# Performance work log

Hardware: AMD Instinct MI355X
Metric: run time of the kernel (lower is better)

Reference implementation:

```python
import jax, jax.numpy as jnp
import numpy as np


def _lstm_cell(x, h, c, w_ih, w_hh, b_ih, b_hh):
    gates = x @ w_ih.T + b_ih + h @ w_hh.T + b_hh  # [B, 4H]
    i, f, g, o = jnp.split(gates, 4, axis=1)
    i = jax.nn.sigmoid(i)
    f = jax.nn.sigmoid(f)
    g = jnp.tanh(g)
    o = jax.nn.sigmoid(o)
    c_next = f * c + i * g
    h_next = o * jnp.tanh(c_next)
    return h_next, c_next


def setup_inputs() -> dict:
    key = jax.random.key(0)
    B, T, D_ENC, H, E, J, V = 32, 512, 512, 640, 640, 640, 4096
    ks = jax.random.split(key, 20)
    s = 0.05
    return {
        "encoder_outputs": jax.random.normal(ks[0], (B, D_ENC, T), jnp.float32),
        "targets": jax.random.randint(ks[1], (B, 1), 0, V, jnp.int64),
        "target_length": jnp.ones((B,), jnp.int32),
        "input_states_1": jax.random.normal(ks[2], (2, B, H), jnp.float32),
        "input_states_2": jax.random.normal(ks[3], (2, B, H), jnp.float32),
        "lstm_w_ih_l0": jax.random.normal(ks[4], (4 * H, E), jnp.float32) * s,
        "lstm_w_hh_l0": jax.random.normal(ks[5], (4 * H, H), jnp.float32) * s,
        "lstm_b_ih_l0": jax.random.normal(ks[6], (4 * H,), jnp.float32) * s,
        "lstm_b_hh_l0": jax.random.normal(ks[7], (4 * H,), jnp.float32) * s,
        "lstm_w_ih_l1": jax.random.normal(ks[8], (4 * H, H), jnp.float32) * s,
        "lstm_w_hh_l1": jax.random.normal(ks[9], (4 * H, H), jnp.float32) * s,
        "lstm_b_ih_l1": jax.random.normal(ks[10], (4 * H,), jnp.float32) * s,
        "lstm_b_hh_l1": jax.random.normal(ks[11], (4 * H,), jnp.float32) * s,
        "embed_weight": jax.random.normal(ks[12], (V, E), jnp.float32) * s,
        "joint_enc_weight": jax.random.normal(ks[13], (J, D_ENC), jnp.float32) * s,
        "joint_enc_bias": jax.random.normal(ks[14], (J,), jnp.float32) * s,
        "joint_pred_weight": jax.random.normal(ks[15], (J, H), jnp.float32) * s,
        "joint_pred_bias": jax.random.normal(ks[16], (J,), jnp.float32) * s,
        "joint_out_weight": jax.random.normal(ks[17], (V, J), jnp.float32) * s,
        "joint_out_bias": jax.random.normal(ks[18], (V,), jnp.float32) * s,
    }


def reference(encoder_outputs, targets, target_length, input_states_1, input_states_2,
              lstm_w_ih_l0, lstm_w_hh_l0, lstm_b_ih_l0, lstm_b_hh_l0,
              lstm_w_ih_l1, lstm_w_hh_l1, lstm_b_ih_l1, lstm_b_hh_l1,
              embed_weight, joint_enc_weight, joint_enc_bias,
              joint_pred_weight, joint_pred_bias, joint_out_weight, joint_out_bias):
    tokens = targets.astype(jnp.int64)
    x_t = embed_weight[tokens[:, 0]]  # [B, E] (only first token used)
    h0, c0 = _lstm_cell(x_t, input_states_1[0], input_states_2[0],
                        lstm_w_ih_l0, lstm_w_hh_l0, lstm_b_ih_l0, lstm_b_hh_l0)
    h1, c1 = _lstm_cell(h0, input_states_1[1], input_states_2[1],
                        lstm_w_ih_l1, lstm_w_hh_l1, lstm_b_ih_l1, lstm_b_hh_l1)
    enc = jnp.transpose(encoder_outputs, (0, 2, 1))  # [B, T, D_enc]
    f = enc @ joint_enc_weight.T + joint_enc_bias    # [B, T, J]
    g = h1 @ joint_pred_weight.T + joint_pred_bias   # [B, J] (U=1)
    joint = jax.nn.relu(f[:, :, None, :] + g[:, None, None, :])  # [B, T, 1, J]
    outputs = joint @ joint_out_weight.T + joint_out_bias        # [B, T, 1, V]
    output_states_1 = jnp.stack([h0, h1], axis=0)
    output_states_2 = jnp.stack([c0, c1], axis=0)
    return outputs, target_length, output_states_1, output_states_2
```

## Files before the change

kernel.cpp:

```cpp
#include <hip/hip_runtime.h>
#include <stdint.h>

#define B_  32
#define T_  512
#define DE_ 512
#define H_  640
#define V_  4096
#define J_  640

typedef __attribute__((ext_vector_type(4))) float  f32x4;
typedef __attribute__((ext_vector_type(8))) __bf16 bf16x8;

typedef __attribute__((address_space(3))) void LdsV;
typedef __attribute__((address_space(1))) void GloV;

__device__ __forceinline__ unsigned short f2bf(float f) {
    uint32_t u = __builtin_bit_cast(uint32_t, f);
    u += 0x7fffu + ((u >> 16) & 1u);
    return (unsigned short)(u >> 16);
}

__global__ void conv_f32_bf16_k(const float* __restrict__ src,
                                unsigned short* __restrict__ dst, int n) {
    int i = blockIdx.x * blockDim.x + threadIdx.x;
    if (i < n) dst[i] = f2bf(src[i]);
}

__global__ void enc_transpose_k(const float* __restrict__ enc,
                                unsigned short* __restrict__ out) {
    __shared__ float tile[32][33];
    int b  = blockIdx.z;
    int t0 = blockIdx.x * 32, d0 = blockIdx.y * 32;
    int tx = threadIdx.x & 31;
    int ty = (threadIdx.x >> 5) * 4;
    const float* src = enc + ((size_t)b * DE_ + d0) * T_ + t0;
#pragma unroll
    for (int i = 0; i < 4; i++)
        tile[ty + i][tx] = src[(size_t)(ty + i) * T_ + tx];
    __syncthreads();
    unsigned short* dst = out + ((size_t)b * T_ + t0) * DE_ + d0;
#pragma unroll
    for (int i = 0; i < 4; i++)
        dst[(size_t)(ty + i) * DE_ + tx] = f2bf(tile[tx][ty + i]);
}

__global__ void lstm_gates_k(const float* __restrict__ x, const int* __restrict__ tok,
                             const float* __restrict__ emb, const float* __restrict__ h,
                             const float* __restrict__ wih, const float* __restrict__ whh,
                             const float* __restrict__ bih, const float* __restrict__ bhh,
                             float* __restrict__ gates) {
    int n = blockIdx.x, lane = threadIdx.x;
    float wi[10], wh[10];
#pragma unroll
    for (int i = 0; i < 10; i++) {
        wi[i] = wih[(size_t)n * H_ + lane + 64 * i];
        wh[i] = whh[(size_t)n * H_ + lane + 64 * i];
    }
    float bias = bih[n] + bhh[n];
    for (int b = 0; b < B_; b++) {
        const float* xr = tok ? (emb + (size_t)tok[b] * H_) : (x + (size_t)b * H_);
        const float* hr = h + (size_t)b * H_;
        float s = 0.f;
#pragma unroll
        for (int i = 0; i < 10; i++)
            s += wi[i] * xr[lane + 64 * i] + wh[i] * hr[lane + 64 * i];
#pragma unroll
        for (int off = 32; off > 0; off >>= 1)
            s += __shfl_down(s, off, 64);
        if (lane == 0) gates[(size_t)b * (4 * H_) + n] = s + bias;
    }
}

__global__ void lstm_update_k(const float* __restrict__ gates, const float* __restrict__ c_in,
                              float* __restrict__ h_out, float* __restrict__ c_out,
                              const int* __restrict__ tlen, float* __restrict__ tlen_out) {
    int idx = blockIdx.x * blockDim.x + threadIdx.x;
    if (tlen_out != nullptr && idx < B_) tlen_out[idx] = (float)tlen[idx];
    if (idx >= B_ * H_) return;
    int b = idx / H_, j = idx - b * H_;
    const float* gr = gates + (size_t)b * 4 * H_;
    float ig = 1.f / (1.f + expf(-gr[j]));
    float fg = 1.f / (1.f + expf(-gr[H_ + j]));
    float gg = tanhf(gr[2 * H_ + j]);
    float og = 1.f / (1.f + expf(-gr[3 * H_ + j]));
    float c  = fg * c_in[idx] + ig * gg;
    h_out[idx] = og * tanhf(c);
    c_out[idx] = c;
}

__global__ void pred_g_k(const float* __restrict__ h1, const float* __restrict__ wp,
                         const float* __restrict__ bp, float* __restrict__ g) {
    int j = blockIdx.x, lane = threadIdx.x;
    float w[10];
#pragma unroll
    for (int i = 0; i < 10; i++) w[i] = wp[(size_t)j * H_ + lane + 64 * i];
    for (int b = 0; b < B_; b++) {
        const float* hr = h1 + (size_t)b * H_;
        float s = 0.f;
#pragma unroll
        for (int i = 0; i < 10; i++) s += w[i] * hr[lane + 64 * i];
#pragma unroll
        for (int off = 32; off > 0; off >>= 1)
            s += __shfl_down(s, off, 64);
        if (lane == 0) g[(size_t)b * J_ + j] = s + bp[j];
    }
}

template <int K, int EPI>
__global__ __launch_bounds__(256) void gemm_bt_k(
        const unsigned short* __restrict__ A, const unsigned short* __restrict__ Bm,
        const float* __restrict__ bias, const float* __restrict__ g,
        float* __restrict__ outF, unsigned short* __restrict__ outU, int ldn) {
    __shared__ __align__(16) unsigned short As[128 * 32];
    __shared__ __align__(16) unsigned short Bs[128 * 32];
    const int tid  = threadIdx.x;
    const int w    = tid >> 6;
    const int lane = tid & 63;
    const int tile_n = blockIdx.x * 128;
    const int tile_m = blockIdx.y * 128;
    const int wm = w & 1, wn = w >> 1;
    const int l15 = lane & 15, quad = lane >> 4;
    const int lr = lane >> 2, lc = lane & 3;

    f32x4 zero = {0.f, 0.f, 0.f, 0.f};
    f32x4 acc[4][4];
#pragma unroll
    for (int i = 0; i < 4; i++)
#pragma unroll
        for (int j = 0; j < 4; j++) acc[i][j] = zero;

    for (int k0 = 0; k0 < K; k0 += 32) {
#pragma unroll
        for (int cc = 0; cc < 2; cc++) {
            const int c = 2 * w + cc;
            const char* ga = (const char*)(A + (size_t)(tile_m + 16 * c + lr) * K)
                             + (size_t)k0 * 2 + lc * 16;
            __builtin_amdgcn_global_load_lds((const GloV*)ga,
                    (LdsV*)((char*)As + c * 1024), 16, 0, 0);
            const char* gb = (const char*)(Bm + (size_t)(tile_n + 16 * c + lr) * K)
                             + (size_t)k0 * 2 + lc * 16;
            __builtin_amdgcn_global_load_lds((const GloV*)gb,
                    (LdsV*)((char*)Bs + c * 1024), 16, 0, 0);
        }
        __syncthreads();

        bf16x8 av[4], bv[4];
#pragma unroll
        for (int i = 0; i < 4; i++) {
            av[i] = *(const bf16x8*)&As[(wm * 64 + i * 16 + l15) * 32 + quad * 8];
            bv[i] = *(const bf16x8*)&Bs[(wn * 64 + i * 16 + l15) * 32 + quad * 8];
        }
#pragma unroll
        for (int i = 0; i < 4; i++)
#pragma unroll
            for (int j = 0; j < 4; j++)
                acc[i][j] = __builtin_amdgcn_mfma_f32_16x16x32_bf16(av[i], bv[j], acc[i][j], 0, 0, 0);
        __syncthreads();
    }

#pragma unroll
    for (int i = 0; i < 4; i++) {
        const int mb = tile_m + wm * 64 + i * 16 + quad * 4;
#pragma unroll
        for (int j = 0; j < 4; j++) {
            const int n = tile_n + wn * 64 + j * 16 + l15;
#pragma unroll
            for (int r = 0; r < 4; r++) {
                float v = acc[i][j][r] + bias[n];
                if (EPI == 0) {
                    outF[(size_t)(mb + r) * ldn + n] = v;
                } else {
                    v += g[(size_t)((mb + r) >> 9) * J_ + n];
                    outU[(size_t)(mb + r) * ldn + n] = f2bf(fmaxf(v, 0.f));
                }
            }
        }
    }
}

extern "C" void kernel_launch(void* const* d_in, const int* in_sizes, int n_in,
                              void* d_out, int out_size, void* d_ws, size_t ws_size,
                              hipStream_t stream) {
    const float* enc   = (const float*)d_in[0];
    const int*   tgt   = (const int*)d_in[1];
    const int*   tlen  = (const int*)d_in[2];
    const float* st1   = (const float*)d_in[3];
    const float* st2   = (const float*)d_in[4];
    const float* wih0  = (const float*)d_in[5];
    const float* whh0  = (const float*)d_in[6];
    const float* bih0  = (const float*)d_in[7];
    const float* bhh0  = (const float*)d_in[8];
    const float* wih1  = (const float*)d_in[9];
    const float* whh1  = (const float*)d_in[10];
    const float* bih1  = (const float*)d_in[11];
    const float* bhh1  = (const float*)d_in[12];
    const float* emb   = (const float*)d_in[13];
    const float* wenc  = (const float*)d_in[14];
    const float* benc  = (const float*)d_in[15];
    const float* wpred = (const float*)d_in[16];
    const float* bpred = (const float*)d_in[17];
    const float* wout  = (const float*)d_in[18];
    const float* bout  = (const float*)d_in[19];

    float* out      = (float*)d_out;
    float* out_tlen = out + (size_t)B_ * T_ * V_;
    float* h0 = out_tlen + B_;
    float* h1 = h0 + B_ * H_;
    float* c0 = h1 + B_ * H_;
    float* c1 = c0 + B_ * H_;

    unsigned short* encB  = (unsigned short*)d_ws;
    unsigned short* pB    = encB + (size_t)B_ * T_ * DE_;
    unsigned short* woutB = pB + (size_t)B_ * T_ * J_;
    unsigned short* wencB = woutB + (size_t)V_ * J_;
    float* gates = (float*)(wencB + (size_t)J_ * DE_);
    float* gvec  = gates + B_ * 4 * H_;

    conv_f32_bf16_k<<<(V_ * J_ + 255) / 256, 256, 0, stream>>>(wout, woutB, V_ * J_);
    conv_f32_bf16_k<<<(J_ * DE_ + 255) / 256, 256, 0, stream>>>(wenc, wencB, J_ * DE_);
    enc_transpose_k<<<dim3(T_ / 32, DE_ / 32, B_), 256, 0, stream>>>(enc, encB);

    lstm_gates_k<<<4 * H_, 64, 0, stream>>>(nullptr, tgt, emb, st1, wih0, whh0, bih0, bhh0, gates);
    lstm_update_k<<<(B_ * H_ + 255) / 256, 256, 0, stream>>>(gates, st2, h0, c0, tlen, out_tlen);
    lstm_gates_k<<<4 * H_, 64, 0, stream>>>(h0, nullptr, nullptr, st1 + B_ * H_, wih1, whh1, bih1, bhh1, gates);
    lstm_update_k<<<(B_ * H_ + 255) / 256, 256, 0, stream>>>(gates, st2 + B_ * H_, h1, c1, nullptr, nullptr);
    pred_g_k<<<J_, 64, 0, stream>>>(h1, wpred, bpred, gvec);

    gemm_bt_k<DE_, 1><<<dim3(J_ / 128, (B_ * T_) / 128), 256, 0, stream>>>(
        encB, wencB, benc, gvec, nullptr, pB, J_);
    gemm_bt_k<J_, 0><<<dim3(V_ / 128, (B_ * T_) / 128), 256, 0, stream>>>(
        pB, woutB, bout, nullptr, out, nullptr, V_);
}
```

Before: 536.1 us.

## Fuse LSTM gate and update kernels, merge conversions, swizzle output GEMM tiles

Merges the two weight-conversion launches into one kernel and folds the LSTM gate GEMV and pointwise update into a single kernel per layer, computing all four gates for one hidden unit per wave. The target-length copy moves into the prediction kernel, which now packs four outputs per block. The output GEMM gains an XCD-aware block-index swizzle so neighbouring tiles share L2 on the same die. Together these cut launch count and the gates round trip through memory, at the cost of more registers per thread in the fused LSTM kernel.

```diff
diff --git a/kernel.cpp b/kernel.cpp
--- a/kernel.cpp
+++ b/kernel.cpp
@@ -20,10 +20,13 @@
     return (unsigned short)(u >> 16);
 }
 
-__global__ void conv_f32_bf16_k(const float* __restrict__ src,
-                                unsigned short* __restrict__ dst, int n) {
+__global__ void conv2_f32_bf16_k(const float* __restrict__ s1, int n1,
+                                 const float* __restrict__ s2, int n2,
+                                 unsigned short* __restrict__ d1,
+                                 unsigned short* __restrict__ d2) {
     int i = blockIdx.x * blockDim.x + threadIdx.x;
-    if (i < n) dst[i] = f2bf(src[i]);
+    if (i < n1) d1[i] = f2bf(s1[i]);
+    else if (i - n1 < n2) d2[i - n1] = f2bf(s2[i - n1]);
 }
 
 __global__ void enc_transpose_k(const float* __restrict__ enc,
@@ -44,56 +47,69 @@
         dst[(size_t)(ty + i) * DE_ + tx] = f2bf(tile[tx][ty + i]);
 }
 
-__global__ void lstm_gates_k(const float* __restrict__ x, const int* __restrict__ tok,
-                             const float* __restrict__ emb, const float* __restrict__ h,
+__global__ void lstm_fused_k(const float* __restrict__ x, const int* __restrict__ tok,
+                             const float* __restrict__ emb,
+                             const float* __restrict__ hprev, const float* __restrict__ cprev,
                              const float* __restrict__ wih, const float* __restrict__ whh,
                              const float* __restrict__ bih, const float* __restrict__ bhh,
-                             float* __restrict__ gates) {
-    int n = blockIdx.x, lane = threadIdx.x;
-    float wi[10], wh[10];
-#pragma unroll
-    for (int i = 0; i < 10; i++) {
-        wi[i] = wih[(size_t)n * H_ + lane + 64 * i];
-        wh[i] = whh[(size_t)n * H_ + lane + 64 * i];
-    }
-    float bias = bih[n] + bhh[n];
+                             float* __restrict__ h_out, float* __restrict__ c_out) {
+    const int j    = blockIdx.x * 4 + (threadIdx.x >> 6);
+    const int lane = threadIdx.x & 63;
+    float wi[4][10], wh[4][10];
+#pragma unroll
+    for (int g = 0; g < 4; g++)
+#pragma unroll
+        for (int i = 0; i < 10; i++) {
+            wi[g][i] = wih[(size_t)(g * H_ + j) * H_ + lane + 64 * i];
+            wh[g][i] = whh[(size_t)(g * H_ + j) * H_ + lane + 64 * i];
+        }
+    float bias[4];
+#pragma unroll
+    for (int g = 0; g < 4; g++) bias[g] = bih[g * H_ + j] + bhh[g * H_ + j];
+
     for (int b = 0; b < B_; b++) {
         const float* xr = tok ? (emb + (size_t)tok[b] * H_) : (x + (size_t)b * H_);
-        const float* hr = h + (size_t)b * H_;
-        float s = 0.f;
-#pragma unroll
-        for (int i = 0; i < 10; i++)
-            s += wi[i] * xr[lane + 64 * i] + wh[i] * hr[lane + 64 * i];
-#pragma unroll
-        for (int off = 32; off > 0; off >>= 1)
-            s += __shfl_down(s, off, 64);
-        if (lane == 0) gates[(size_t)b * (4 * H_) + n] = s + bias;
-    }
-}
-
-__global__ void lstm_update_k(const float* __restrict__ gates, const float* __restrict__ c_in,
-                              float* __restrict__ h_out, float* __restrict__ c_out,
-                              const int* __restrict__ tlen, float* __restrict__ tlen_out) {
-    int idx = blockIdx.x * blockDim.x + threadIdx.x;
-    if (tlen_out != nullptr && idx < B_) tlen_out[idx] = (float)tlen[idx];
-    if (idx >= B_ * H_) return;
-    int b = idx / H_, j = idx - b * H_;
-    const float* gr = gates + (size_t)b * 4 * H_;
-    float ig = 1.f / (1.f + expf(-gr[j]));
-    float fg = 1.f / (1.f + expf(-gr[H_ + j]));
-    float gg = tanhf(gr[2 * H_ + j]);
-    float og = 1.f / (1.f + expf(-gr[3 * H_ + j]));
-    float c  = fg * c_in[idx] + ig * gg;
-    h_out[idx] = og * tanhf(c);
-    c_out[idx] = c;
+        const float* hr = hprev + (size_t)b * H_;
+        float xv[10], hv[10];
+#pragma unroll
+        for (int i = 0; i < 10; i++) { xv[i] = xr[lane + 64 * i]; hv[i] = hr[lane + 64 * i]; }
+        float s0 = 0.f, s1 = 0.f, s2 = 0.f, s3 = 0.f;
+#pragma unroll
+        for (int i = 0; i < 10; i++) {
+            s0 += wi[0][i] * xv[i] + wh[0][i] * hv[i];
+            s1 += wi[1][i] * xv[i] + wh[1][i] * hv[i];
+            s2 += wi[2][i] * xv[i] + wh[2][i] * hv[i];
+            s3 += wi[3][i] * xv[i] + wh[3][i] * hv[i];
+        }
+#pragma unroll
+        for (int off = 32; off > 0; off >>= 1) {
+            s0 += __shfl_down(s0, off, 64);
+            s1 += __shfl_down(s1, off, 64);
+            s2 += __shfl_down(s2, off, 64);
+            s3 += __shfl_down(s3, off, 64);
+        }
+        if (lane == 0) {
+            float ig = 1.f / (1.f + expf(-(s0 + bias[0])));
+            float fg = 1.f / (1.f + expf(-(s1 + bias[1])));
+            float gg = tanhf(s2 + bias[2]);
+            float og = 1.f / (1.f + expf(-(s3 + bias[3])));
+            float c  = fg * cprev[(size_t)b * H_ + j] + ig * gg;
+            c_out[(size_t)b * H_ + j] = c;
+            h_out[(size_t)b * H_ + j] = og * tanhf(c);
+        }
+    }
 }
 
 __global__ void pred_g_k(const float* __restrict__ h1, const float* __restrict__ wp,
-                         const float* __restrict__ bp, float* __restrict__ g) {
-    int j = blockIdx.x, lane = threadIdx.x;
+                         const float* __restrict__ bp, float* __restrict__ g,
+                         const int* __restrict__ tlen, float* __restrict__ tlen_out) {
+    if (blockIdx.x == 0 && threadIdx.x < B_) tlen_out[threadIdx.x] = (float)tlen[threadIdx.x];
+    const int j    = blockIdx.x * 4 + (threadIdx.x >> 6);
+    const int lane = threadIdx.x & 63;
     float w[10];
 #pragma unroll
     for (int i = 0; i < 10; i++) w[i] = wp[(size_t)j * H_ + lane + 64 * i];
+    float bj = bp[j];
     for (int b = 0; b < B_; b++) {
         const float* hr = h1 + (size_t)b * H_;
         float s = 0.f;
@@ -102,22 +118,30 @@
 #pragma unroll
         for (int off = 32; off > 0; off >>= 1)
             s += __shfl_down(s, off, 64);
-        if (lane == 0) g[(size_t)b * J_ + j] = s + bp[j];
-    }
-}
-
-template <int K, int EPI>
+        if (lane == 0) g[(size_t)b * J_ + j] = s + bj;
+    }
+}
+
+template <int K, int EPI, int SWZ>
 __global__ __launch_bounds__(256) void gemm_bt_k(
         const unsigned short* __restrict__ A, const unsigned short* __restrict__ Bm,
         const float* __restrict__ bias, const float* __restrict__ g,
         float* __restrict__ outF, unsigned short* __restrict__ outU, int ldn) {
-    __shared__ __align__(16) unsigned short As[128 * 32];
-    __shared__ __align__(16) unsigned short Bs[128 * 32];
+    __shared__ __align__(16) unsigned short SMEM[2 * 128 * 32];
+    unsigned short* As = SMEM;
+    unsigned short* Bs = SMEM + 128 * 32;
     const int tid  = threadIdx.x;
     const int w    = tid >> 6;
     const int lane = tid & 63;
-    const int tile_n = blockIdx.x * 128;
-    const int tile_m = blockIdx.y * 128;
+    int bx = blockIdx.x, by = blockIdx.y;
+    if (SWZ) {
+        int L = by * 32 + bx;
+        int xcd = L & 7, s = L >> 3;
+        bx = xcd * 4 + (s & 3);
+        by = s >> 2;
+    }
+    const int tile_n = bx * 128;
+    const int tile_m = by * 128;
     const int wm = w & 1, wn = w >> 1;
     const int l15 = lane & 15, quad = lane >> 4;
     const int lr = lane >> 2, lc = lane & 3;
@@ -213,21 +237,20 @@
     unsigned short* pB    = encB + (size_t)B_ * T_ * DE_;
     unsigned short* woutB = pB + (size_t)B_ * T_ * J_;
     unsigned short* wencB = woutB + (size_t)V_ * J_;
-    float* gates = (float*)(wencB + (size_t)J_ * DE_);
-    float* gvec  = gates + B_ * 4 * H_;
-
-    conv_f32_bf16_k<<<(V_ * J_ + 255) / 256, 256, 0, stream>>>(wout, woutB, V_ * J_);
-    conv_f32_bf16_k<<<(J_ * DE_ + 255) / 256, 256, 0, stream>>>(wenc, wencB, J_ * DE_);
+    float* gvec = (float*)(wencB + (size_t)J_ * DE_);
+
+    conv2_f32_bf16_k<<<(V_ * J_ + J_ * DE_ + 255) / 256, 256, 0, stream>>>(
+        wout, V_ * J_, wenc, J_ * DE_, woutB, wencB);
     enc_transpose_k<<<dim3(T_ / 32, DE_ / 32, B_), 256, 0, stream>>>(enc, encB);
 
-    lstm_gates_k<<<4 * H_, 64, 0, stream>>>(nullptr, tgt, emb, st1, wih0, whh0, bih0, bhh0, gates);
-    lstm_update_k<<<(B_ * H_ + 255) / 256, 256, 0, stream>>>(gates, st2, h0, c0, tlen, out_tlen);
-    lstm_gates_k<<<4 * H_, 64, 0, stream>>>(h0, nullptr, nullptr, st1 + B_ * H_, wih1, whh1, bih1, bhh1, gates);
-    lstm_update_k<<<(B_ * H_ + 255) / 256, 256, 0, stream>>>(gates, st2 + B_ * H_, h1, c1, nullptr, nullptr);
-    pred_g_k<<<J_, 64, 0, stream>>>(h1, wpred, bpred, gvec);
-
-    gemm_bt_k<DE_, 1><<<dim3(J_ / 128, (B_ * T_) / 128), 256, 0, stream>>>(
+    lstm_fused_k<<<H_ / 4, 256, 0, stream>>>(nullptr, tgt, emb, st1, st2,
+                                             wih0, whh0, bih0, bhh0, h0, c0);
+    lstm_fused_k<<<H_ / 4, 256, 0, stream>>>(h0, nullptr, nullptr, st1 + B_ * H_, st2 + B_ * H_,
+                                             wih1, whh1, bih1, bhh1, h1, c1);
+    pred_g_k<<<H_ / 4, 256, 0, stream>>>(h1, wpred, bpred, gvec, tlen, out_tlen);
+
+    gemm_bt_k<DE_, 1, 0><<<dim3(J_ / 128, (B_ * T_) / 128), 256, 0, stream>>>(
         encB, wencB, benc, gvec, nullptr, pB, J_);
-    gemm_bt_k<J_, 0><<<dim3(V_ / 128, (B_ * T_) / 128), 256, 0, stream>>>(
+    gemm_bt_k<J_, 0, 1><<<dim3(V_ / 128, (B_ * T_) / 128), 256, 0, stream>>>(
         pB, woutB, bout, nullptr, out, nullptr, V_);
 }
```

Result: slower. 588.9 us (+9.9%).
